# Optimization experiments

Measured on AMD Instinct MI355X. Metric: run time of the kernel, lower is better.

Reference implementation:

```python
import jax, jax.numpy as jnp
import numpy as np

SOS = 4999
EOS = 4999
SCALING = 2.0  # ESPnet AttDot softmax scaling
NEG = -1e30


def setup_inputs() -> dict:
    key = jax.random.key(0)
    ks = jax.random.split(key, 12)
    B, T, E, D, V, L = 32, 400, 1024, 1024, 5000, 100
    s = lambda k, shape: (jax.random.normal(k, shape, jnp.float32) * 0.02)
    return dict(
        hs_pad=jax.random.normal(ks[0], (B, T, E), jnp.float32),
        embed=s(ks[1], (V, D)),
        Wenc=s(ks[2], (D, E)), benc=jnp.zeros((D,), jnp.float32),
        Wdec=s(ks[3], (D, D)), bdec=jnp.zeros((D,), jnp.float32),
        W_ih0=s(ks[4], (4 * D, D + E)), W_hh0=s(ks[5], (4 * D, D)),
        b_ih0=jnp.zeros((4 * D,), jnp.float32), b_hh0=jnp.zeros((4 * D,), jnp.float32),
        W_ih1=s(ks[6], (4 * D, D)), W_hh1=s(ks[7], (4 * D, D)),
        b_ih1=jnp.zeros((4 * D,), jnp.float32), b_hh1=jnp.zeros((4 * D,), jnp.float32),
        Wout=s(ks[8], (V, D + E)), bout=jnp.zeros((V,), jnp.float32),
        hlens=jax.random.randint(ks[9], (B,), T // 2, T + 1, jnp.int32),
        ys_pad=jax.random.randint(ks[10], (B, L), 0, V - 1, jnp.int64),
    )


def lstm_cell(x, h, c, W_ih, W_hh, b_ih, b_hh):
    # torch.nn.LSTMCell gate order: i, f, g, o
    g = x @ W_ih.T + b_ih + h @ W_hh.T + b_hh
    i, f, gg, o = jnp.split(g, 4, axis=-1)
    c2 = jax.nn.sigmoid(f) * c + jax.nn.sigmoid(i) * jnp.tanh(gg)
    h2 = jax.nn.sigmoid(o) * jnp.tanh(c2)
    return h2, c2


def reference(hs_pad, embed, Wenc, benc, Wdec, bdec,
              W_ih0, W_hh0, b_ih0, b_hh0, W_ih1, W_hh1, b_ih1, b_hh1,
              Wout, bout, hlens, ys_pad):
    B, T, E = hs_pad.shape
    V, D = embed.shape
    L = ys_pad.shape[1]
    # teacher forcing sequences: ys_in = [sos; y], ys_out = [y; eos]
    sos_col = jnp.full((B, 1), SOS, ys_pad.dtype)
    eos_col = jnp.full((B, 1), EOS, ys_pad.dtype)
    ys_in = jnp.concatenate([sos_col, ys_pad], axis=1)   # [B, L+1]
    ys_out = jnp.concatenate([ys_pad, eos_col], axis=1)  # [B, L+1]
    eys = embed[ys_in]                                   # [B, L+1, D]

    # AttDot precompute: tanh(W_enc h)
    pre_enc = jnp.tanh(jnp.einsum('bte,de->btd', hs_pad, Wenc) + benc)  # [B,T,D]
    mask = jnp.arange(T)[None, :] < hlens[:, None]                      # [B,T]

    def step(carry, ey):
        z0, c0, z1, c1 = carry
        dq = jnp.tanh(z0 @ Wdec.T + bdec)                    # [B,D]
        e = jnp.einsum('btd,bd->bt', pre_enc, dq)            # [B,T]
        e = jnp.where(mask, SCALING * e, NEG)
        w = jax.nn.softmax(e, axis=-1)
        att_c = jnp.einsum('bt,bte->be', w, hs_pad)          # [B,E]
        x = jnp.concatenate([ey, att_c], axis=-1)            # [B,D+E]
        z0, c0 = lstm_cell(x, z0, c0, W_ih0, W_hh0, b_ih0, b_hh0)
        z1, c1 = lstm_cell(z0, z1, c1, W_ih1, W_hh1, b_ih1, b_hh1)
        z_sc = jnp.concatenate([z1, att_c], axis=-1)         # [B,D+E]
        return (z0, c0, z1, c1), z_sc

    zeros = jnp.zeros((B, D), hs_pad.dtype)
    _, z_all = jax.lax.scan(step, (zeros, zeros, zeros, zeros),
                            jnp.swapaxes(eys, 0, 1))         # [L+1,B,D+E]
    y_all = jnp.einsum('lbd,vd->lbv', z_all, Wout) + bout    # [L+1,B,V]
    logp = jax.nn.log_softmax(y_all, axis=-1)
    tgt = ys_out.T                                           # [L+1,B]
    ce = -jnp.take_along_axis(logp, tgt[..., None], axis=-1)[..., 0]
    # loss = mean CE * (mean(len ys_in) - 1) = mean CE * L (no padding)
    loss = ce.mean() * jnp.asarray(L, ce.dtype)
    return loss
```

## Files before the change

### kernel.cpp

```cpp
#include <hip/hip_runtime.h>
#include <cstdint>
#include <cstddef>


using short8  = __attribute__((ext_vector_type(8))) short;
using floatx4 = __attribute__((ext_vector_type(4))) float;
using floatx2 = __attribute__((ext_vector_type(2))) float;
typedef unsigned long long u64;

#define DEV __device__ __forceinline__

#if defined(__has_builtin)
#if __has_builtin(__builtin_amdgcn_cvt_pk_f32_fp8) && __has_builtin(__builtin_amdgcn_cvt_pk_fp8_f32)
#define HW_FP8 1
#endif
#endif

DEV float bf2f(unsigned int h) { union { unsigned int u; float f; } v; v.u = h << 16; return v.f; }
DEV unsigned short f2bf(float f) {
    union { float f; unsigned int u; } v; v.f = f;
    return (unsigned short)((v.u + 0x7fffu + ((v.u >> 16) & 1u)) >> 16);
}
DEV float sigm(float x) { return 1.0f / (1.0f + __expf(-x)); }

DEV float fp8tof_sw(unsigned int b) {
    unsigned int s = (b & 0x80u) << 24;
    unsigned int em = b & 0x7fu;
    float vn = __uint_as_float(s | ((em + 960u) << 20));
    float vd = (float)(int)em * 0x1p-9f;
    vd = s ? -vd : vd;
    return (em >= 8u) ? vn : vd;
}
DEV unsigned int f2fp8_sw(float f) {
    unsigned int u = __float_as_uint(f);
    unsigned int s = (u >> 24) & 0x80u;
    unsigned int a = u & 0x7fffffffu;
    if (a >= 0x43e00000u) return s | 0x7eu;
    if (a < 0x3c800000u) {
        unsigned int mi = (unsigned int)(__uint_as_float(a) * 512.0f + 0.5f);
        return s | mi;
    }
    unsigned int lsb = (a >> 20) & 1u;
    a += 0x0007ffffu + lsb;
    unsigned int e = (a >> 23) - 120u;
    unsigned int m = (a >> 20) & 7u;
    return s | (e << 3) | m;
}
DEV void un4(unsigned int w, float* o) {
#ifdef HW_FP8
    floatx2 lo = __builtin_amdgcn_cvt_pk_f32_fp8((int)w, false);
    floatx2 hi = __builtin_amdgcn_cvt_pk_f32_fp8((int)w, true);
    o[0] = lo.x; o[1] = lo.y; o[2] = hi.x; o[3] = hi.y;
#else
    o[0] = fp8tof_sw(w & 0xffu); o[1] = fp8tof_sw((w >> 8) & 0xffu);
    o[2] = fp8tof_sw((w >> 16) & 0xffu); o[3] = fp8tof_sw(w >> 24);
#endif
}
DEV unsigned int pack4fp8(float a, float b, float c, float d) {
#ifdef HW_FP8
    int w = __builtin_amdgcn_cvt_pk_fp8_f32(a, b, 0, false);
    w = __builtin_amdgcn_cvt_pk_fp8_f32(c, d, w, true);
    return (unsigned int)w;
#else
    return f2fp8_sw(a) | (f2fp8_sw(b) << 8) | (f2fp8_sw(c) << 16) | (f2fp8_sw(d) << 24);
#endif
}
DEV unsigned char f2fp8_1(float v) {
#ifdef HW_FP8
    return (unsigned char)((unsigned int)__builtin_amdgcn_cvt_pk_fp8_f32(v, v, 0, false) & 0xffu);
#else
    return (unsigned char)f2fp8_sw(v);
#endif
}
DEV u64 pack4bf16(float a, float b, float c, float d) {
    union { unsigned int w[2]; u64 q; } u;
    u.w[0] = (unsigned int)f2bf(a) | ((unsigned int)f2bf(b) << 16);
    u.w[1] = (unsigned int)f2bf(c) | ((unsigned int)f2bf(d) << 16);
    return u.q;
}

DEV u64  lda64(const void* p) { return __hip_atomic_load((const u64*)p, __ATOMIC_RELAXED, __HIP_MEMORY_SCOPE_AGENT); }
DEV void sta64(void* p, u64 v) { __hip_atomic_store((u64*)p, v, __ATOMIC_RELAXED, __HIP_MEMORY_SCOPE_AGENT); }
DEV void sta32(void* p, unsigned int v) { __hip_atomic_store((unsigned int*)p, v, __ATOMIC_RELAXED, __HIP_MEMORY_SCOPE_AGENT); }
DEV float ldaf(const void* p) { return __hip_atomic_load((const float*)p, __ATOMIC_RELAXED, __HIP_MEMORY_SCOPE_AGENT); }
DEV void staf(void* p, float v) { __hip_atomic_store((float*)p, v, __ATOMIC_RELAXED, __HIP_MEMORY_SCOPE_AGENT); }
DEV int  arrive(int* p) { return __hip_atomic_fetch_add(p, 1, __ATOMIC_RELAXED, __HIP_MEMORY_SCOPE_AGENT); }

__global__ __launch_bounds__(256) void k_zero(unsigned int* p, int n) {
    int i = blockIdx.x * 256 + threadIdx.x;
    if (i < n) p[i] = 0u;
}

__global__ __launch_bounds__(256) void k_conv4(const float* __restrict__ in,
                                               unsigned short* __restrict__ out, int n4) {
    int i = blockIdx.x * 256 + threadIdx.x;
    if (i >= n4) return;
    float4 v = ((const float4*)in)[i];
    unsigned int w0 = (unsigned int)f2bf(v.x) | ((unsigned int)f2bf(v.y) << 16);
    unsigned int w1 = (unsigned int)f2bf(v.z) | ((unsigned int)f2bf(v.w) << 16);
    ((uint2*)(void*)out)[i] = make_uint2(w0, w1);
}

__global__ __launch_bounds__(256) void k_convhs(const float* __restrict__ in,
                                                unsigned short* __restrict__ obf,
                                                unsigned int* __restrict__ o8, int n4) {
    int i = blockIdx.x * 256 + threadIdx.x;
    if (i >= n4) return;
    float4 v = ((const float4*)in)[i];
    unsigned int w0 = (unsigned int)f2bf(v.x) | ((unsigned int)f2bf(v.y) << 16);
    unsigned int w1 = (unsigned int)f2bf(v.z) | ((unsigned int)f2bf(v.w) << 16);
    ((uint2*)(void*)obf)[i] = make_uint2(w0, w1);
    o8[i] = pack4fp8(v.x, v.y, v.z, v.w);
}

__global__ __launch_bounds__(256) void k_conv8(const float* __restrict__ in,
                                               unsigned int* __restrict__ o8, int n4) {
    int i = blockIdx.x * 256 + threadIdx.x;
    if (i >= n4) return;
    float4 v = ((const float4*)in)[i];
    o8[i] = pack4fp8(v.x, v.y, v.z, v.w);
}

__global__ __launch_bounds__(256) void k_catp8(const float* __restrict__ A, const float* __restrict__ Bsrc,
                                               unsigned int* __restrict__ dst, int Ka, int Kb) {
    int idx = blockIdx.x * 256 + threadIdx.x;
    int K4 = (Ka + Kb) >> 2;
    if (idx >= 4096 * K4) return;
    int n = idx / K4, k4 = idx - n * K4, k = k4 * 4;
    const float* src = (k < Ka) ? (A + (size_t)n * Ka + k) : (Bsrc + (size_t)n * Kb + (k - Ka));
    int outrow = ((n & 1023) >> 2) * 16 + (n >> 10) * 4 + (n & 3);
    dst[(size_t)outrow * K4 + k4] = pack4fp8(src[0], src[1], src[2], src[3]);
}

__global__ __launch_bounds__(256) void k_woutpad(const float* __restrict__ W, unsigned short* __restrict__ dst) {
    int idx = blockIdx.x * 256 + threadIdx.x;
    if (idx >= 5120 * 2048) return;
    int n = idx >> 11, k = idx & 2047;
    dst[idx] = (n < 5000) ? f2bf(W[(size_t)n * 2048 + k]) : (unsigned short)0;
}

__global__ __launch_bounds__(256) void k_bsum(const float* a0, const float* b0, const float* a1, const float* b1,
                                              float* s0, float* s1) {
    int i = blockIdx.x * 256 + threadIdx.x;
    if (i < 4096) s0[i] = a0[i] + b0[i];
    else if (i < 8192) s1[i - 4096] = a1[i - 4096] + b1[i - 4096];
}

__global__ __launch_bounds__(256) void k_eys8(const float* __restrict__ embed, const int* __restrict__ ys_pad,
                                              unsigned int* __restrict__ eys8) {
    int idx = blockIdx.x * 256 + threadIdx.x;
    if (idx >= 3232 * 256) return;
    int rb = idx >> 8, c4 = idx & 255;
    int l = rb >> 5, b = rb & 31;
    int tok = (l == 0) ? 4999 : ys_pad[b * 100 + (l - 1)];
    const float* e = embed + (size_t)tok * 1024 + c4 * 4;
    eys8[idx] = pack4fp8(e[0], e[1], e[2], e[3]);
}

__global__ __launch_bounds__(256) void k_dq0(const float* __restrict__ bdec, unsigned short* __restrict__ dq) {
    int idx = blockIdx.x * 256 + threadIdx.x;
    if (idx >= 32768) return;
    dq[idx] = f2bf(tanhf(bdec[idx & 1023]));
}

__global__ __launch_bounds__(256) void k_gemm128(
    const unsigned short* __restrict__ A, const unsigned short* __restrict__ B,
    int K, int N, const float* __restrict__ bias,
    unsigned char* __restrict__ o8, float* __restrict__ of32, int mode) {
    __shared__ uint4 Ab[512];
    __shared__ uint4 Bb[512];
    const int tid = threadIdx.x;
    const int lane = tid & 63, wave = tid >> 6;
    const int r = lane & 15, q = lane >> 4;
    const int wm = wave >> 1, wn = wave & 1;
    const size_t am0 = (size_t)blockIdx.y * 128;
    const size_t bn0 = (size_t)blockIdx.x * 128;
    floatx4 zf = {0.f, 0.f, 0.f, 0.f};
    floatx4 acc[4][4];
#pragma unroll
    for (int i = 0; i < 4; i++)
#pragma unroll
        for (int j = 0; j < 4; j++) acc[i][j] = zf;

    for (int k0 = 0; k0 < K; k0 += 32) {
        __syncthreads();
#pragma unroll
        for (int i = 0; i < 2; ++i) {
            int idx = i * 256 + tid;
            int qq = idx & 3, rr = idx >> 2;
            int slot = (rr >> 4) * 64 + ((qq << 4) | (rr & 15));
            Ab[slot] = *(const uint4*)(const void*)(A + (am0 + rr) * K + k0 + qq * 8);
            Bb[slot] = *(const uint4*)(const void*)(B + (bn0 + rr) * K + k0 + qq * 8);
        }
        __syncthreads();
        short8 af[4], bf[4];
#pragma unroll
        for (int t = 0; t < 4; t++) af[t] = *(const short8*)(const void*)&Ab[(wm * 4 + t) * 64 + lane];
#pragma unroll
        for (int t = 0; t < 4; t++) bf[t] = *(const short8*)(const void*)&Bb[(wn * 4 + t) * 64 + lane];
#pragma unroll
        for (int tm = 0; tm < 4; tm++)
#pragma unroll
            for (int tn = 0; tn < 4; tn++)
                acc[tm][tn] = __builtin_amdgcn_mfma_f32_16x16x32_bf16(af[tm], bf[tn], acc[tm][tn], 0, 0, 0);
    }
#pragma unroll
    for (int tm = 0; tm < 4; tm++) {
#pragma unroll
        for (int tn = 0; tn < 4; tn++) {
            int col = (int)bn0 + wn * 64 + tn * 16 + r;
#pragma unroll
            for (int reg = 0; reg < 4; ++reg) {
                size_t row = am0 + wm * 64 + tm * 16 + q * 4 + reg;
                float v = acc[tm][tn][reg];
                if (mode == 0) {
                    v = tanhf(v + bias[col]);
                    o8[row * (size_t)N + col] = f2fp8_1(v);
                } else {
                    of32[row * (size_t)N + col] = v;
                }
            }
        }
    }
}

struct SArgs {
    const unsigned char* pre8;
    const unsigned char* hs8;
    const unsigned char* eys8;
    const unsigned char* wc0p;
    const unsigned char* wc1p;
    const unsigned char* wdec;
    unsigned short* dq;
    unsigned char* attp;
    unsigned char* z0p;
    unsigned char* z1p;
    unsigned short* zall;
    const float* bdec; const float* bs0; const float* bs1;
    float* part; float* lmaxg; float* lsumg;
    int* cntA; int* gcnt; int* gflag;
    const int* hlens;
};

DEV void gbar(int* gcnt, int* gflag, int ep, int grp) {
    __builtin_amdgcn_s_waitcnt(0);
    __syncthreads();
    if (threadIdx.x == 0) {
        int old = arrive(gcnt + grp * 32);
        if (old == ep * 32 - 1) {
            int o2 = arrive(gcnt + 256);
            if (o2 == ep * 8 - 1) {
                __hip_atomic_store(gflag, ep, __ATOMIC_RELAXED, __HIP_MEMORY_SCOPE_AGENT);
            }
        }
        while (__hip_atomic_load(gflag, __ATOMIC_RELAXED, __HIP_MEMORY_SCOPE_AGENT) < ep)
            __builtin_amdgcn_s_sleep(1);
    }
    __syncthreads();
}

__global__ __launch_bounds__(256, 1) void k_scan(SArgs a) {
    const int blk = blockIdx.x, tid = threadIdx.x;
    const int lane = tid & 63, wave = tid >> 6;
    const int b = blk >> 3, ch = blk & 7;
    const int dc = blk;
    const int grp = blk & 7;
    const int r = lane & 15, q = lane >> 4;
    const int hlen = a.hlens[b];

    __shared__ __align__(16) unsigned char hsS[51200];
    __shared__ __align__(16) unsigned char xS[32 * 3088];
    __shared__ __align__(16) float redS[4][64][8];
    __shared__ float e4[50][4];
    __shared__ float es[52];
    __shared__ float ps[52];
    __shared__ float c0S[4][32], c1S[4][32];
    __shared__ unsigned char  z8tmp[128];
    __shared__ unsigned short z16tmp[128];
    __shared__ unsigned short dq16tmp[128];
    __shared__ int lastf;

    {
        const u64* hsrc = (const u64*)(const void*)(a.hs8 + (size_t)(b * 400 + ch * 50) * 1024);
        u64* hd = (u64*)(void*)hsS;
        for (int i = tid; i < 6400; i += 256) hd[i] = hsrc[i];
        if (tid < 128) { c0S[tid >> 5][tid & 31] = 0.f; c1S[tid >> 5][tid & 31] = 0.f; }
    }
    __syncthreads();

    int ep = 0;
    for (int l = 0; l < 101; ++l) {
        unsigned char* z0cur = a.z0p + (size_t)(l & 1) * 32768;
        unsigned char* z0prv = a.z0p + (size_t)((l + 1) & 1) * 32768;
        unsigned char* z1cur = a.z1p + (size_t)(l & 1) * 32768;
        unsigned char* z1prv = a.z1p + (size_t)((l + 1) & 1) * 32768;

        {
            ((u64*)(void*)xS)[tid] = lda64((const char*)(const void*)a.dq + (size_t)b * 2048 + tid * 8);
            __syncthreads();
            float dqf[16];
            {
                const unsigned int* dw = (const unsigned int*)(const void*)xS + lane * 8;
#pragma unroll
                for (int i = 0; i < 8; ++i) {
                    unsigned int w = dw[i];
                    dqf[2 * i] = bf2f(w & 0xffffu);
                    dqf[2 * i + 1] = bf2f(w >> 16);
                }
            }
            const uint4* prow = (const uint4*)(const void*)(a.pre8 + (size_t)(b * 400 + ch * 50) * 1024);
            for (int tl = wave; tl < 50; tl += 4) {
                uint4 v = prow[tl * 64 + lane];
                float x[16];
                un4(v.x, x); un4(v.y, x + 4); un4(v.z, x + 8); un4(v.w, x + 12);
                float s = 0.f;
#pragma unroll
                for (int i = 0; i < 16; ++i) s += x[i] * dqf[i];
                s += __shfl_xor(s, 1, 64);
                s += __shfl_xor(s, 2, 64);
                s += __shfl_xor(s, 4, 64);
                s += __shfl_xor(s, 8, 64);
                if ((lane & 15) == 0) e4[tl][lane >> 4] = s;
            }
            __syncthreads();
            if (tid < 50) {
                float4 v = *(const float4*)(const void*)e4[tid];
                float e = v.x + v.y + v.z + v.w;
                int t = ch * 50 + tid;
                es[tid] = (t < hlen) ? 2.0f * e : -1e30f;
            }
            __syncthreads();
            float lmax = -1e30f;
#pragma unroll
            for (int i = 0; i < 50; ++i) lmax = fmaxf(lmax, es[i]);
            if (tid < 50) ps[tid] = (es[tid] > -5e29f) ? __expf(es[tid] - lmax) : 0.f;
            __syncthreads();
            if (tid == 0) {
                float ssum = 0.f;
                for (int i = 0; i < 50; ++i) ssum += ps[i];
                staf(a.lmaxg + b * 8 + ch, lmax);
                staf(a.lsumg + b * 8 + ch, ssum);
            }
            const int c = tid * 4;
            float a0 = 0.f, a1 = 0.f, a2 = 0.f, a3 = 0.f;
            for (int tl = 0; tl < 50; ++tl) {
                float p = ps[tl];
                unsigned int h = *(const unsigned int*)(const void*)(hsS + tl * 1024 + c);
                float x[4];
                un4(h, x);
                a0 += p * x[0]; a1 += p * x[1]; a2 += p * x[2]; a3 += p * x[3];
            }
            {
                float* pb = a.part + ((size_t)(b * 8 + ch)) * 1024 + c;
                union { float f[2]; u64 q; } p0, p1;
                p0.f[0] = a0; p0.f[1] = a1; p1.f[0] = a2; p1.f[1] = a3;
                sta64(pb, p0.q); sta64(pb + 2, p1.q);
            }
            __builtin_amdgcn_s_waitcnt(0);
            __syncthreads();
            if (tid == 0) lastf = (arrive(a.cntA + b * 32) == 8 * l + 7);
            __syncthreads();
            if (lastf) {
                float lm[8], ls[8];
#pragma unroll
                for (int i = 0; i < 8; ++i) {
                    lm[i] = ldaf(a.lmaxg + b * 8 + i);
                    ls[i] = ldaf(a.lsumg + b * 8 + i);
                }
                float gm = -1e30f;
#pragma unroll
                for (int i = 0; i < 8; ++i) gm = fmaxf(gm, lm[i]);
                float Zs = 0.f;
#pragma unroll
                for (int i = 0; i < 8; ++i) Zs += ls[i] * __expf(lm[i] - gm);
                const float inv = 1.0f / Zs;
                float o0 = 0.f, o1 = 0.f, o2 = 0.f, o3 = 0.f;
#pragma unroll
                for (int i = 0; i < 8; ++i) {
                    float coef = __expf(lm[i] - gm) * inv;
                    const float* qp = a.part + ((size_t)(b * 8 + i)) * 1024 + c;
                    union { u64 q; float f[2]; } u0, u1;
                    u0.q = lda64(qp); u1.q = lda64(qp + 2);
                    o0 += coef * u0.f[0]; o1 += coef * u0.f[1];
                    o2 += coef * u1.f[0]; o3 += coef * u1.f[1];
                }
                sta32(a.attp + (size_t)b * 1024 + c, pack4fp8(o0, o1, o2, o3));
                sta64(a.zall + ((size_t)(l * 32 + b)) * 2048 + 1024 + c, pack4bf16(o0, o1, o2, o3));
            }
        }
        gbar(a.gcnt, a.gflag, ++ep, grp);

        {
            {
                const uint4* ey = (const uint4*)(const void*)(a.eys8 + (size_t)l * 32768);
                for (int i = tid; i < 2048; i += 256) {
                    int row = i >> 6, off = i & 63;
                    *(uint4*)(void*)&xS[row * 3088 + off * 16] = ey[row * 64 + off];
                }
                for (int i = tid; i < 4096; i += 256) {
                    int row = i >> 7, off = i & 127;
                    *(u64*)(void*)&xS[row * 3088 + 1024 + off * 8] = lda64(a.attp + (size_t)row * 1024 + off * 8);
                }
                for (int i = tid; i < 4096; i += 256) {
                    int row = i >> 7, off = i & 127;
                    *(u64*)(void*)&xS[row * 3088 + 2048 + off * 8] = lda64(z0prv + (size_t)row * 1024 + off * 8);
                }
            }
            __syncthreads();
            const unsigned char* Br = a.wc0p + ((size_t)(dc * 16 + r)) * 3072 + wave * 768 + q * 8;
            const unsigned char* A0 = &xS[r * 3088 + wave * 768 + q * 8];
            const unsigned char* A1 = A0 + 16 * 3088;
            floatx4 acc0 = {0.f, 0.f, 0.f, 0.f}, acc1 = acc0;
#pragma unroll 8
            for (int kk = 0; kk < 768; kk += 32) {
                long long bfr = *(const long long*)(const void*)(Br + kk);
                long long a0 = *(const long long*)(const void*)(A0 + kk);
                long long a1 = *(const long long*)(const void*)(A1 + kk);
                acc0 = __builtin_amdgcn_mfma_f32_16x16x32_fp8_fp8(a0, bfr, acc0, 0, 0, 0);
                acc1 = __builtin_amdgcn_mfma_f32_16x16x32_fp8_fp8(a1, bfr, acc1, 0, 0, 0);
            }
            *(floatx4*)(void*)&redS[wave][lane][0] = acc0;
            *(floatx4*)(void*)&redS[wave][lane][4] = acc1;
            __syncthreads();
            if (tid < 128) {
                const int bb = tid & 31, j = tid >> 5;
                const int qp = (bb & 15) >> 2;
                const int slot = (bb & 3) + ((bb >> 4) << 2);
                float g[4];
#pragma unroll
                for (int gg = 0; gg < 4; ++gg) {
                    const int lp = (qp << 4) | (gg * 4 + j);
                    g[gg] = redS[0][lp][slot] + redS[1][lp][slot] + redS[2][lp][slot] + redS[3][lp][slot]
                          + a.bs0[gg * 1024 + dc * 4 + j];
                }
                float cn = sigm(g[1]) * c0S[j][bb] + sigm(g[0]) * tanhf(g[2]);
                c0S[j][bb] = cn;
                float z = sigm(g[3]) * tanhf(cn);
                z8tmp[bb * 4 + j] = f2fp8_1(z);
            }
            __syncthreads();
            if (tid < 32) {
                unsigned int w = *(const unsigned int*)(const void*)&z8tmp[tid * 4];
                sta32(z0cur + (size_t)tid * 1024 + dc * 4, w);
            }
        }
        gbar(a.gcnt, a.gflag, ++ep, grp);

        {
            for (int i = tid; i < 4096; i += 256) {
                int row = i >> 7, off = i & 127;
                *(u64*)(void*)&xS[row * 2064 + off * 8] = lda64(z0cur + (size_t)row * 1024 + off * 8);
            }
            for (int i = tid; i < 4096; i += 256) {
                int row = i >> 7, off = i & 127;
                *(u64*)(void*)&xS[row * 2064 + 1024 + off * 8] = lda64(z1prv + (size_t)row * 1024 + off * 8);
            }
            __syncthreads();
            {
                const unsigned char* Br = a.wc1p + ((size_t)(dc * 16 + r)) * 2048 + wave * 512 + q * 8;
                const unsigned char* A0 = &xS[r * 2064 + wave * 512 + q * 8];
                const unsigned char* A1 = A0 + 16 * 2064;
                floatx4 acc0 = {0.f, 0.f, 0.f, 0.f}, acc1 = acc0;
#pragma unroll 8
                for (int kk = 0; kk < 512; kk += 32) {
                    long long bfr = *(const long long*)(const void*)(Br + kk);
                    long long a0 = *(const long long*)(const void*)(A0 + kk);
                    long long a1 = *(const long long*)(const void*)(A1 + kk);
                    acc0 = __builtin_amdgcn_mfma_f32_16x16x32_fp8_fp8(a0, bfr, acc0, 0, 0, 0);
                    acc1 = __builtin_amdgcn_mfma_f32_16x16x32_fp8_fp8(a1, bfr, acc1, 0, 0, 0);
                }
                *(floatx4*)(void*)&redS[wave][lane][0] = acc0;
                *(floatx4*)(void*)&redS[wave][lane][4] = acc1;
            }
            __syncthreads();
            if (tid < 128) {
                const int bb = tid & 31, j = tid >> 5;
                const int qp = (bb & 15) >> 2;
                const int slot = (bb & 3) + ((bb >> 4) << 2);
                float g[4];
#pragma unroll
                for (int gg = 0; gg < 4; ++gg) {
                    const int lp = (qp << 4) | (gg * 4 + j);
                    g[gg] = redS[0][lp][slot] + redS[1][lp][slot] + redS[2][lp][slot] + redS[3][lp][slot]
                          + a.bs1[gg * 1024 + dc * 4 + j];
                }
                float cn = sigm(g[1]) * c1S[j][bb] + sigm(g[0]) * tanhf(g[2]);
                c1S[j][bb] = cn;
                float z = sigm(g[3]) * tanhf(cn);
                z8tmp[bb * 4 + j] = f2fp8_1(z);
                z16tmp[bb * 4 + j] = f2bf(z);
            }
            __syncthreads();
            {
                const unsigned char* Bd = a.wdec + ((size_t)(dc * 4 + (r & 3))) * 1024 + wave * 256 + q * 8;
                const unsigned char* D0 = &xS[r * 2064 + wave * 256 + q * 8];
                const unsigned char* D1 = D0 + 16 * 2064;
                floatx4 acc0 = {0.f, 0.f, 0.f, 0.f}, acc1 = acc0;
#pragma unroll 8
                for (int kk = 0; kk < 256; kk += 32) {
                    long long bfr = *(const long long*)(const void*)(Bd + kk);
                    long long a0 = *(const long long*)(const void*)(D0 + kk);
                    long long a1 = *(const long long*)(const void*)(D1 + kk);
                    acc0 = __builtin_amdgcn_mfma_f32_16x16x32_fp8_fp8(a0, bfr, acc0, 0, 0, 0);
                    acc1 = __builtin_amdgcn_mfma_f32_16x16x32_fp8_fp8(a1, bfr, acc1, 0, 0, 0);
                }
                *(floatx4*)(void*)&redS[wave][lane][0] = acc0;
                *(floatx4*)(void*)&redS[wave][lane][4] = acc1;
            }
            __syncthreads();
            if (tid < 128) {
                const int bb = tid & 31, j = tid >> 5;
                const int qp = (bb & 15) >> 2;
                const int slot = (bb & 3) + ((bb >> 4) << 2);
                const int lp = (qp << 4) | j;
                float s = redS[0][lp][slot] + redS[1][lp][slot] + redS[2][lp][slot] + redS[3][lp][slot];
                dq16tmp[bb * 4 + j] = f2bf(tanhf(s + a.bdec[dc * 4 + j]));
            }
            __syncthreads();
            if (tid < 32) {
                unsigned int wz = *(const unsigned int*)(const void*)&z8tmp[tid * 4];
                sta32(z1cur + (size_t)tid * 1024 + dc * 4, wz);
                u64 wq = *(const u64*)(const void*)&z16tmp[tid * 4];
                sta64(a.zall + ((size_t)(l * 32 + tid)) * 2048 + dc * 4, wq);
                u64 wd = *(const u64*)(const void*)&dq16tmp[tid * 4];
                sta64((char*)(void*)a.dq + (size_t)tid * 2048 + dc * 8, wd);
            }
        }
        gbar(a.gcnt, a.gflag, ++ep, grp);
    }
}

__global__ __launch_bounds__(256) void k_ce(const float* __restrict__ y, const float* __restrict__ bout,
                                            const int* __restrict__ ys_pad, float* __restrict__ out) {
    const int rrow = blockIdx.x;
    const int l = rrow >> 5, b = rrow & 31;
    const float* yp = y + (size_t)rrow * 5120;
    const int tid = threadIdx.x;
    __shared__ float red[256];
    float m = -1e30f;
    for (int c = tid; c < 5000; c += 256) m = fmaxf(m, yp[c] + bout[c]);
    red[tid] = m; __syncthreads();
    for (int s = 128; s; s >>= 1) { if (tid < s) red[tid] = fmaxf(red[tid], red[tid + s]); __syncthreads(); }
    const float gmax = red[0]; __syncthreads();
    float ss = 0.f;
    for (int c = tid; c < 5000; c += 256) ss += __expf(yp[c] + bout[c] - gmax);
    red[tid] = ss; __syncthreads();
    for (int s = 128; s; s >>= 1) { if (tid < s) red[tid] += red[tid + s]; __syncthreads(); }
    if (tid == 0) {
        const int tgt = (l < 100) ? ys_pad[b * 100 + l] : 4999;
        const float lt = yp[tgt] + bout[tgt];
        const float ce = logf(red[0]) + gmax - lt;
        atomicAdd(out, ce * (100.0f / 3232.0f));
    }
}

extern "C" void kernel_launch(void* const* d_in, const int* in_sizes, int n_in,
                              void* d_out, int out_size, void* d_ws, size_t ws_size,
                              hipStream_t stream) {
    const float* hs_pad = (const float*)d_in[0];
    const float* embed  = (const float*)d_in[1];
    const float* Wenc   = (const float*)d_in[2];
    const float* benc   = (const float*)d_in[3];
    const float* Wdec   = (const float*)d_in[4];
    const float* bdec   = (const float*)d_in[5];
    const float* W_ih0  = (const float*)d_in[6];
    const float* W_hh0  = (const float*)d_in[7];
    const float* b_ih0  = (const float*)d_in[8];
    const float* b_hh0  = (const float*)d_in[9];
    const float* W_ih1  = (const float*)d_in[10];
    const float* W_hh1  = (const float*)d_in[11];
    const float* b_ih1  = (const float*)d_in[12];
    const float* b_hh1  = (const float*)d_in[13];
    const float* Wout   = (const float*)d_in[14];
    const float* bout   = (const float*)d_in[15];
    const int*   hlens  = (const int*)d_in[16];
    const int*   ys_pad = (const int*)d_in[17];
    float* out = (float*)d_out;
    uint8_t* ws = (uint8_t*)d_ws;

    constexpr size_t OFF_HS    = 0;
    constexpr size_t OFF_PRE8  = OFF_HS    + 26214400;
    constexpr size_t OFF_HS8   = OFF_PRE8  + 13107200;
    constexpr size_t OFF_WC0P  = OFF_HS8   + 13107200;
    constexpr size_t OFF_WC1P  = OFF_WC0P  + 12582912;
    constexpr size_t OFF_WDEC8 = OFF_WC1P  + 8388608;
    constexpr size_t OFF_WENC  = OFF_WDEC8 + 1048576;
    constexpr size_t OFF_EYS8  = OFF_WENC  + 2097152;
    constexpr size_t OFF_ZALL  = OFF_EYS8  + 3309568;
    constexpr size_t OFF_WOUT  = OFF_ZALL  + 13631488;
    constexpr size_t OFF_PART  = OFF_WOUT  + 20971520;
    constexpr size_t OFF_DQP   = OFF_PART  + 1048576;
    constexpr size_t OFF_ATTP  = OFF_DQP   + 65536;
    constexpr size_t OFF_Z0P   = OFF_ATTP  + 32768;
    constexpr size_t OFF_Z1P   = OFF_Z0P   + 65536;
    constexpr size_t OFF_LMAX  = OFF_Z1P   + 65536;
    constexpr size_t OFF_LSUM  = OFF_LMAX  + 1024;
    constexpr size_t OFF_BS0   = OFF_LSUM  + 1024;
    constexpr size_t OFF_BS1   = OFF_BS0   + 16384;
    constexpr size_t OFF_CNT   = OFF_BS1   + 16384;
    constexpr size_t OFF_Y     = 0;

    unsigned short* HS    = (unsigned short*)(ws + OFF_HS);
    unsigned char*  PRE8  = (unsigned char*)(ws + OFF_PRE8);
    unsigned char*  HS8   = (unsigned char*)(ws + OFF_HS8);
    unsigned char*  WC0P  = (unsigned char*)(ws + OFF_WC0P);
    unsigned char*  WC1P  = (unsigned char*)(ws + OFF_WC1P);
    unsigned char*  WDEC8 = (unsigned char*)(ws + OFF_WDEC8);
    unsigned short* WENC  = (unsigned short*)(ws + OFF_WENC);
    unsigned char*  EYS8  = (unsigned char*)(ws + OFF_EYS8);
    unsigned short* ZALL  = (unsigned short*)(ws + OFF_ZALL);
    unsigned short* WOUTP = (unsigned short*)(ws + OFF_WOUT);
    float* PART  = (float*)(ws + OFF_PART);
    unsigned short* DQP = (unsigned short*)(ws + OFF_DQP);
    unsigned char*  ATTP = (unsigned char*)(ws + OFF_ATTP);
    unsigned char*  Z0P = (unsigned char*)(ws + OFF_Z0P);
    unsigned char*  Z1P = (unsigned char*)(ws + OFF_Z1P);
    float* LMAX  = (float*)(ws + OFF_LMAX);
    float* LSUM  = (float*)(ws + OFF_LSUM);
    float* BS0  = (float*)(ws + OFF_BS0);
    float* BS1  = (float*)(ws + OFF_BS1);
    int* CNT    = (int*)(ws + OFF_CNT);
    float* Y = (float*)(ws + OFF_Y);

    auto Zr = [&](void* p, int n_u32) {
        k_zero<<<dim3((n_u32 + 255) / 256), dim3(256), 0, stream>>>((unsigned int*)p, n_u32);
    };

    Zr(Z0P, 16384);
    Zr(Z1P, 16384);
    Zr(CNT, 2048);
    Zr(d_out, 1);
    Zr(ZALL + (size_t)3232 * 2048, 98304);

    k_convhs<<<dim3(12800), dim3(256), 0, stream>>>(hs_pad, HS, (unsigned int*)(void*)HS8, 3276800);
    k_conv4<<<dim3(1024),  dim3(256), 0, stream>>>(Wenc, WENC, 262144);
    k_conv8<<<dim3(1024),  dim3(256), 0, stream>>>(Wdec, (unsigned int*)(void*)WDEC8, 262144);
    k_catp8<<<dim3(12288), dim3(256), 0, stream>>>(W_ih0, W_hh0, (unsigned int*)(void*)WC0P, 2048, 1024);
    k_catp8<<<dim3(8192),  dim3(256), 0, stream>>>(W_ih1, W_hh1, (unsigned int*)(void*)WC1P, 1024, 1024);
    k_woutpad<<<dim3(40960), dim3(256), 0, stream>>>(Wout, WOUTP);
    k_bsum<<<dim3(32), dim3(256), 0, stream>>>(b_ih0, b_hh0, b_ih1, b_hh1, BS0, BS1);
    k_eys8<<<dim3(3232), dim3(256), 0, stream>>>(embed, ys_pad, (unsigned int*)(void*)EYS8);

    k_gemm128<<<dim3(8, 100), dim3(256), 0, stream>>>(HS, WENC, 1024, 1024, benc, PRE8, (float*)nullptr, 0);
    k_dq0<<<dim3(128), dim3(256), 0, stream>>>(bdec, DQP);

    SArgs sa;
    sa.pre8 = PRE8; sa.hs8 = HS8; sa.eys8 = EYS8;
    sa.wc0p = WC0P; sa.wc1p = WC1P; sa.wdec = WDEC8;
    sa.dq = DQP; sa.attp = ATTP; sa.z0p = Z0P; sa.z1p = Z1P; sa.zall = ZALL;
    sa.bdec = bdec; sa.bs0 = BS0;  sa.bs1 = BS1;
    sa.part = PART; sa.lmaxg = LMAX; sa.lsumg = LSUM;
    sa.cntA = CNT;
    sa.gcnt = CNT + 1024;
    sa.gflag = CNT + 1536;
    sa.hlens = hlens;
    void* kp[] = { &sa };
    hipLaunchCooperativeKernel((const void*)k_scan, dim3(256), dim3(256), kp, 0, stream);

    k_gemm128<<<dim3(40, 26), dim3(256), 0, stream>>>(ZALL, WOUTP, 2048, 5120, (const float*)nullptr,
                                                      (unsigned char*)nullptr, Y, 1);
    k_ce<<<dim3(3232), dim3(256), 0, stream>>>(Y, bout, ys_pad, out);
}
```

Measured before the change: 4.629 ms.

## Cache pre_enc slice in LDS and stream LSTM operands directly from global

Each persistent block now loads its 50-row slice of the precomputed encoder projection into shared memory once, instead of re-reading it from global memory on every decoder step. The shared x staging buffer is dropped, and the LSTM and Wdec MFMA loops read their activation fragments (embeddings, attention context, z0, z1) straight from global or L2 with 8-byte loads. This removes per-step staging copies and two block barriers per phase, and frees LDS for the pre_enc cache. In exchange, activation fragments are re-fetched from global by every block, and the MFMAs now wait on global load latency instead of shared memory reads.

```diff
diff --git a/kernel.cpp b/kernel.cpp
--- a/kernel.cpp
+++ b/kernel.cpp
@@ -268,8 +268,9 @@
     const int r = lane & 15, q = lane >> 4;
     const int hlen = a.hlens[b];
 
+    __shared__ __align__(16) unsigned char preS[51200];
     __shared__ __align__(16) unsigned char hsS[51200];
-    __shared__ __align__(16) unsigned char xS[32 * 3088];
+    __shared__ __align__(16) u64 dqStage[256];
     __shared__ __align__(16) float redS[4][64][8];
     __shared__ float e4[50][4];
     __shared__ float es[52];
@@ -281,9 +282,11 @@
     __shared__ int lastf;
 
     {
+        const u64* psrc = (const u64*)(const void*)(a.pre8 + (size_t)(b * 400 + ch * 50) * 1024);
         const u64* hsrc = (const u64*)(const void*)(a.hs8 + (size_t)(b * 400 + ch * 50) * 1024);
+        u64* pd = (u64*)(void*)preS;
         u64* hd = (u64*)(void*)hsS;
-        for (int i = tid; i < 6400; i += 256) hd[i] = hsrc[i];
+        for (int i = tid; i < 6400; i += 256) { pd[i] = psrc[i]; hd[i] = hsrc[i]; }
         if (tid < 128) { c0S[tid >> 5][tid & 31] = 0.f; c1S[tid >> 5][tid & 31] = 0.f; }
     }
     __syncthreads();
@@ -296,11 +299,11 @@
         unsigned char* z1prv = a.z1p + (size_t)((l + 1) & 1) * 32768;
 
         {
-            ((u64*)(void*)xS)[tid] = lda64((const char*)(const void*)a.dq + (size_t)b * 2048 + tid * 8);
+            dqStage[tid] = lda64((const char*)(const void*)a.dq + (size_t)b * 2048 + tid * 8);
             __syncthreads();
             float dqf[16];
             {
-                const unsigned int* dw = (const unsigned int*)(const void*)xS + lane * 8;
+                const unsigned int* dw = (const unsigned int*)(const void*)dqStage + lane * 8;
 #pragma unroll
                 for (int i = 0; i < 8; ++i) {
                     unsigned int w = dw[i];
@@ -308,9 +311,8 @@
                     dqf[2 * i + 1] = bf2f(w >> 16);
                 }
             }
-            const uint4* prow = (const uint4*)(const void*)(a.pre8 + (size_t)(b * 400 + ch * 50) * 1024);
             for (int tl = wave; tl < 50; tl += 4) {
-                uint4 v = prow[tl * 64 + lane];
+                uint4 v = *(const uint4*)(const void*)(preS + tl * 1024 + lane * 16);
                 float x[16];
                 un4(v.x, x); un4(v.y, x + 4); un4(v.z, x + 8); un4(v.w, x + 12);
                 float s = 0.f;
@@ -391,31 +393,32 @@
         gbar(a.gcnt, a.gflag, ++ep, grp);
 
         {
-            {
-                const uint4* ey = (const uint4*)(const void*)(a.eys8 + (size_t)l * 32768);
-                for (int i = tid; i < 2048; i += 256) {
-                    int row = i >> 6, off = i & 63;
-                    *(uint4*)(void*)&xS[row * 3088 + off * 16] = ey[row * 64 + off];
-                }
-                for (int i = tid; i < 4096; i += 256) {
-                    int row = i >> 7, off = i & 127;
-                    *(u64*)(void*)&xS[row * 3088 + 1024 + off * 8] = lda64(a.attp + (size_t)row * 1024 + off * 8);
-                }
-                for (int i = tid; i < 4096; i += 256) {
-                    int row = i >> 7, off = i & 127;
-                    *(u64*)(void*)&xS[row * 3088 + 2048 + off * 8] = lda64(z0prv + (size_t)row * 1024 + off * 8);
-                }
-            }
-            __syncthreads();
-            const unsigned char* Br = a.wc0p + ((size_t)(dc * 16 + r)) * 3072 + wave * 768 + q * 8;
-            const unsigned char* A0 = &xS[r * 3088 + wave * 768 + q * 8];
-            const unsigned char* A1 = A0 + 16 * 3088;
+            const unsigned char* Br = a.wc0p + ((size_t)(dc * 16 + r)) * 3072 + wave * 256 + q * 8;
+            const char* eyb  = (const char*)(const void*)a.eys8 + (size_t)l * 32768 + r * 1024 + wave * 256 + q * 8;
+            const char* attb = (const char*)(const void*)a.attp + (size_t)r * 1024 + wave * 256 + q * 8;
+            const char* z0b  = (const char*)(const void*)z0prv + (size_t)r * 1024 + wave * 256 + q * 8;
             floatx4 acc0 = {0.f, 0.f, 0.f, 0.f}, acc1 = acc0;
-#pragma unroll 8
-            for (int kk = 0; kk < 768; kk += 32) {
+#pragma unroll
+            for (int kk = 0; kk < 256; kk += 32) {
                 long long bfr = *(const long long*)(const void*)(Br + kk);
-                long long a0 = *(const long long*)(const void*)(A0 + kk);
-                long long a1 = *(const long long*)(const void*)(A1 + kk);
+                long long a0 = *(const long long*)(const void*)(eyb + kk);
+                long long a1 = *(const long long*)(const void*)(eyb + 16384 + kk);
+                acc0 = __builtin_amdgcn_mfma_f32_16x16x32_fp8_fp8(a0, bfr, acc0, 0, 0, 0);
+                acc1 = __builtin_amdgcn_mfma_f32_16x16x32_fp8_fp8(a1, bfr, acc1, 0, 0, 0);
+            }
+#pragma unroll
+            for (int kk = 0; kk < 256; kk += 32) {
+                long long bfr = *(const long long*)(const void*)(Br + 1024 + kk);
+                long long a0 = (long long)lda64(attb + kk);
+                long long a1 = (long long)lda64(attb + 16384 + kk);
+                acc0 = __builtin_amdgcn_mfma_f32_16x16x32_fp8_fp8(a0, bfr, acc0, 0, 0, 0);
+                acc1 = __builtin_amdgcn_mfma_f32_16x16x32_fp8_fp8(a1, bfr, acc1, 0, 0, 0);
+            }
+#pragma unroll
+            for (int kk = 0; kk < 256; kk += 32) {
+                long long bfr = *(const long long*)(const void*)(Br + 2048 + kk);
+                long long a0 = (long long)lda64(z0b + kk);
+                long long a1 = (long long)lda64(z0b + 16384 + kk);
                 acc0 = __builtin_amdgcn_mfma_f32_16x16x32_fp8_fp8(a0, bfr, acc0, 0, 0, 0);
                 acc1 = __builtin_amdgcn_mfma_f32_16x16x32_fp8_fp8(a1, bfr, acc1, 0, 0, 0);
             }
@@ -447,25 +450,24 @@
         gbar(a.gcnt, a.gflag, ++ep, grp);
 
         {
-            for (int i = tid; i < 4096; i += 256) {
-                int row = i >> 7, off = i & 127;
-                *(u64*)(void*)&xS[row * 2064 + off * 8] = lda64(z0cur + (size_t)row * 1024 + off * 8);
-            }
-            for (int i = tid; i < 4096; i += 256) {
-                int row = i >> 7, off = i & 127;
-                *(u64*)(void*)&xS[row * 2064 + 1024 + off * 8] = lda64(z1prv + (size_t)row * 1024 + off * 8);
-            }
-            __syncthreads();
             {
-                const unsigned char* Br = a.wc1p + ((size_t)(dc * 16 + r)) * 2048 + wave * 512 + q * 8;
-                const unsigned char* A0 = &xS[r * 2064 + wave * 512 + q * 8];
-                const unsigned char* A1 = A0 + 16 * 2064;
+                const unsigned char* Br = a.wc1p + ((size_t)(dc * 16 + r)) * 2048 + wave * 256 + q * 8;
+                const char* z0b = (const char*)(const void*)z0cur + (size_t)r * 1024 + wave * 256 + q * 8;
+                const char* z1b = (const char*)(const void*)z1prv + (size_t)r * 1024 + wave * 256 + q * 8;
                 floatx4 acc0 = {0.f, 0.f, 0.f, 0.f}, acc1 = acc0;
-#pragma unroll 8
-                for (int kk = 0; kk < 512; kk += 32) {
+#pragma unroll
+                for (int kk = 0; kk < 256; kk += 32) {
                     long long bfr = *(const long long*)(const void*)(Br + kk);
-                    long long a0 = *(const long long*)(const void*)(A0 + kk);
-                    long long a1 = *(const long long*)(const void*)(A1 + kk);
+                    long long a0 = (long long)lda64(z0b + kk);
+                    long long a1 = (long long)lda64(z0b + 16384 + kk);
+                    acc0 = __builtin_amdgcn_mfma_f32_16x16x32_fp8_fp8(a0, bfr, acc0, 0, 0, 0);
+                    acc1 = __builtin_amdgcn_mfma_f32_16x16x32_fp8_fp8(a1, bfr, acc1, 0, 0, 0);
+                }
+#pragma unroll
+                for (int kk = 0; kk < 256; kk += 32) {
+                    long long bfr = *(const long long*)(const void*)(Br + 1024 + kk);
+                    long long a0 = (long long)lda64(z1b + kk);
+                    long long a1 = (long long)lda64(z1b + 16384 + kk);
                     acc0 = __builtin_amdgcn_mfma_f32_16x16x32_fp8_fp8(a0, bfr, acc0, 0, 0, 0);
                     acc1 = __builtin_amdgcn_mfma_f32_16x16x32_fp8_fp8(a1, bfr, acc1, 0, 0, 0);
                 }
@@ -493,14 +495,13 @@
             __syncthreads();
             {
                 const unsigned char* Bd = a.wdec + ((size_t)(dc * 4 + (r & 3))) * 1024 + wave * 256 + q * 8;
-                const unsigned char* D0 = &xS[r * 2064 + wave * 256 + q * 8];
-                const unsigned char* D1 = D0 + 16 * 2064;
+                const char* D0 = (const char*)(const void*)z0cur + (size_t)r * 1024 + wave * 256 + q * 8;
                 floatx4 acc0 = {0.f, 0.f, 0.f, 0.f}, acc1 = acc0;
-#pragma unroll 8
+#pragma unroll
                 for (int kk = 0; kk < 256; kk += 32) {
                     long long bfr = *(const long long*)(const void*)(Bd + kk);
-                    long long a0 = *(const long long*)(const void*)(D0 + kk);
-                    long long a1 = *(const long long*)(const void*)(D1 + kk);
+                    long long a0 = (long long)lda64(D0 + kk);
+                    long long a1 = (long long)lda64(D0 + 16384 + kk);
                     acc0 = __builtin_amdgcn_mfma_f32_16x16x32_fp8_fp8(a0, bfr, acc0, 0, 0, 0);
                     acc1 = __builtin_amdgcn_mfma_f32_16x16x32_fp8_fp8(a1, bfr, acc1, 0, 0, 0);
                 }
```

After: 3.847 ms. -16.9%, faster.
